# Performance work log

Hardware: AMD Instinct MI355X
Metric: run time of the kernel (lower is better)

Reference implementation:

```python
import jax, jax.numpy as jnp
import numpy as np

B, DIM, HID, K, G, MID = 1024, 384, 64, 8, 48, 128
EPS = 1e-06


def _gaussian_8x8():
    t = jnp.arange(K, dtype=jnp.float32) - 3.5
    g = jnp.exp(-(t[:, None] ** 2 + t[None, :] ** 2) / (2.0 * 2.0 ** 2))
    return g / g.sum()


def setup_inputs() -> dict:
    key = jax.random.key(0)
    ks = jax.random.split(key, 16)
    inp = {
        "x": jax.random.normal(ks[0], (B, DIM), dtype=jnp.float32),
        "W": jax.random.normal(ks[1], (DIM, HID), dtype=jnp.float32) * 0.02,
        "b": jax.random.normal(ks[2], (DIM, HID), dtype=jnp.float32) * 0.02,
        "patch_weight": _gaussian_8x8(),  # learnable 8x8, softmaxed in forward
        "pair_w1": jax.random.normal(ks[3], (G, G), dtype=jnp.float32) * 0.02,
        "pair_b1": jax.random.normal(ks[4], (G, G), dtype=jnp.float32) * 0.02,
        "pair_w2": jax.random.normal(ks[5], (G, G), dtype=jnp.float32) * 0.02,
        "pair_b2": jax.random.normal(ks[6], (G, G), dtype=jnp.float32) * 0.02,
        # nn.Linear(G, DIM)
        "proj_w": jax.random.normal(ks[7], (DIM, G), dtype=jnp.float32) * (1.0 / np.sqrt(G)),
        "proj_b": jax.random.normal(ks[8], (DIM,), dtype=jnp.float32) * 0.02,
        # nn.Linear(HID, MID)
        "down_w": jax.random.normal(ks[9], (MID, HID), dtype=jnp.float32) * (1.0 / np.sqrt(HID)),
        "down_b": jax.random.normal(ks[10], (MID,), dtype=jnp.float32) * 0.02,
        # nn.Linear(MID, HID)
        "up_w": jax.random.normal(ks[11], (HID, MID), dtype=jnp.float32) * (1.0 / np.sqrt(MID)),
        "up_b": jax.random.normal(ks[12], (HID,), dtype=jnp.float32) * 0.02,
    }
    return inp


def _leaky(v):
    return jnp.where(v >= 0, v, 0.01 * v)


def reference(x, W, b, patch_weight, pair_w1, pair_b1, pair_w2, pair_b2,
              proj_w, proj_b, down_w, down_b, up_w, up_b):
    # scale / inverse-bias GELU features: (B, DIM, HID)
    s = x[:, :, None]
    inv = 1.0 / (jnp.abs(s) + EPS)
    H = jax.nn.gelu(s * W[None] + inv * b[None], approximate=False)
    # Gram matrix over hidden dim: (B, DIM, DIM)
    P = jnp.einsum('bik,bjk->bij', H, H)
    # learnable gaussian patch pooling (softmax over flattened 8x8 weights)
    w = jax.nn.softmax(patch_weight.reshape(-1)).reshape(K, K)
    Pg = jnp.einsum('bgkhl,kl->bgh', P.reshape(-1, G, K, G, K), w)  # (B, G, G)
    # two elementwise gated leaky layers
    Pg = _leaky(Pg * pair_w1[None] + pair_b1[None])
    Pg = _leaky(Pg * pair_w2[None] + pair_b2[None])
    # softmax + nonlinear row reduction -> (B, G)
    row_soft = jax.nn.softmax(Pg, axis=-1)
    row_weights = (1.0 / (1.0 + row_soft ** 2)).sum(axis=-1)
    # project 48 -> 384, scale rows of H
    scales = row_weights @ proj_w.T + proj_b  # (B, DIM)
    H = H * scales[:, :, None]
    # tiny MLP on hidden dim
    z = _leaky(H @ down_w.T + down_b)
    z = _leaky(z @ up_w.T + up_b)
    return z
```

## Files before the change

kernel.cpp:

```cpp
#include <hip/hip_runtime.h>


#define EPSF 1e-6f

typedef __attribute__((ext_vector_type(8))) short bf16x8;
typedef __attribute__((ext_vector_type(4))) float f32x4;
typedef __attribute__((ext_vector_type(4))) unsigned short u16x4;

__device__ __forceinline__ unsigned short f2bf(float f) {
    union { float f; unsigned int u; } v; v.f = f;
    unsigned int r = v.u + 0x7fffu + ((v.u >> 16) & 1u);
    return (unsigned short)(r >> 16);
}
__device__ __forceinline__ float bf2f(unsigned short h) {
    union { unsigned int u; float f; } v; v.u = ((unsigned int)h) << 16;
    return v.f;
}
__device__ __forceinline__ float leaky(float v) { return fmaxf(v, 0.01f * v); }
__device__ __forceinline__ int key8(int r) { return (r ^ (r >> 3)) & 7; }
__device__ __forceinline__ float gelu_f(float u) {
    float t = u * (1.5957691216f + 0.0713548163f * (u * u));
    float e = __expf(t);
    float r = __builtin_amdgcn_rcpf(e + 1.0f);
    return fmaf(-u, r, u);
}

__global__ void prep(const float* __restrict__ proj_w,
                     const float* __restrict__ down_w,
                     const float* __restrict__ up_w,
                     float* __restrict__ ws) {
    int idx = blockIdx.x * blockDim.x + threadIdx.x;
    unsigned short* wb = (unsigned short*)(ws + 18432);
    if (idx < 18432) {
        int i = idx / 48, g = idx % 48;
        ws[g * 384 + i] = proj_w[idx];
    } else if (idx < 26624) {
        int k = idx - 18432;
        wb[k] = f2bf(down_w[k]);
    } else if (idx < 34816) {
        int k = idx - 26624;
        wb[8192 + k] = f2bf(up_w[k]);
    }
}

__global__ __launch_bounds__(512, 4) void pg_scales(
    const float* __restrict__ x,
    const float* __restrict__ W,
    const float* __restrict__ bb,
    const float* __restrict__ patch_weight,
    const float* __restrict__ pw1, const float* __restrict__ pb1,
    const float* __restrict__ pw2, const float* __restrict__ pb2,
    const float* __restrict__ proj_b,
    float* __restrict__ ws)
{
    __shared__ __align__(16) unsigned short sH[24576];
    __shared__ __align__(16) unsigned short sRB[12288];
    __shared__ float sw[64];
    __shared__ float srw[48];

    const int t = threadIdx.x;
    const int b = blockIdx.x;
    const int wv = t >> 6, lane = t & 63, q = lane >> 4, r = lane & 15;
    const float* projT = ws;
    float* scales_g = ws + 26624;
    unsigned short* sM  = sRB;
    float* sPg = (float*)sRB;

    if (t < 64) {
        float p = patch_weight[t];
        float m = p;
        for (int o = 32; o > 0; o >>= 1) m = fmaxf(m, __shfl_xor(m, o));
        float e = __expf(p - m);
        float s = e;
        for (int o = 32; o > 0; o >>= 1) s += __shfl_xor(s, o);
        sw[t] = e * __builtin_amdgcn_rcpf(s);
    }

    for (int j = 0; j < 12; ++j) {
        int idx4 = j * 512 + t;
        int base = idx4 * 4;
        int i = base >> 6, c0 = base & 63;
        float4 w4 = ((const float4*)W)[idx4];
        float4 b4 = ((const float4*)bb)[idx4];
        float xi  = x[b * 384 + i];
        float inv = __builtin_amdgcn_rcpf(fabsf(xi) + EPSF);
        u16x4 hv;
        hv[0] = f2bf(gelu_f(fmaf(xi, w4.x, inv * b4.x)));
        hv[1] = f2bf(gelu_f(fmaf(xi, w4.y, inv * b4.y)));
        hv[2] = f2bf(gelu_f(fmaf(xi, w4.z, inv * b4.z)));
        hv[3] = f2bf(gelu_f(fmaf(xi, w4.w, inv * b4.w)));
        int cb = c0 >> 3, cc = c0 & 7;
        *(u16x4*)&sH[i * 64 + ((cb ^ key8(i)) << 3) + cc] = hv;
    }
    __syncthreads();

    f32x4 pacc  = {0.f, 0.f, 0.f, 0.f};
    f32x4 pacc8 = {0.f, 0.f, 0.f, 0.f};
    for (int hc = 0; hc < 2; ++hc) {
        if (t < 384) {
            const int cb = t & 3, lq = (t >> 2) & 1, g = t >> 3;
            float acc[4][8];
            #pragma unroll
            for (int a = 0; a < 4; ++a)
                #pragma unroll
                for (int cc = 0; cc < 8; ++cc) acc[a][cc] = 0.0f;
            #pragma unroll
            for (int k = 0; k < 8; ++k) {
                int i = g * 8 + k;
                int cbh = hc * 4 + cb;
                bf16x8 hv = *(const bf16x8*)&sH[i * 64 + ((cbh ^ key8(i)) << 3)];
                f32x4 w4 = *(const f32x4*)&sw[k * 8 + lq * 4];
                float hf[8];
                #pragma unroll
                for (int cc = 0; cc < 8; ++cc) hf[cc] = bf2f((unsigned short)hv[cc]);
                #pragma unroll
                for (int a = 0; a < 4; ++a)
                    #pragma unroll
                    for (int cc = 0; cc < 8; ++cc)
                        acc[a][cc] = fmaf(w4[a], hf[cc], acc[a][cc]);
            }
            #pragma unroll
            for (int a = 0; a < 4; ++a) {
                int l = lq * 4 + a;
                int cbl = l * 4 + cb;
                int cbs = (cbl & 24) | ((cbl ^ key8(g)) & 7);
                bf16x8 mv;
                #pragma unroll
                for (int cc = 0; cc < 8; ++cc) mv[cc] = (short)f2bf(acc[a][cc]);
                *(bf16x8*)&sM[g * 256 + (cbs << 3)] = mv;
            }
        }
        __syncthreads();
        {
            const int tg = wv / 3, th = wv % 3;
            #pragma unroll
            for (int ks = 0; ks < 8; ++ks) {
                int g = tg * 16 + r;
                int cbl = ks * 4 + q;
                int cbs = (cbl & 24) | ((cbl ^ key8(g)) & 7);
                bf16x8 av = *(const bf16x8*)&sM[g * 256 + (cbs << 3)];
                int i = (th * 16 + r) * 8 + ks;
                int cbh = hc * 4 + q;
                bf16x8 bv = *(const bf16x8*)&sH[i * 64 + ((cbh ^ key8(i)) << 3)];
                pacc = __builtin_amdgcn_mfma_f32_16x16x32_bf16(av, bv, pacc, 0, 0, 0);
            }
            if (wv == 7) {
                #pragma unroll
                for (int ks = 0; ks < 8; ++ks) {
                    int g = 32 + r;
                    int cbl = ks * 4 + q;
                    int cbs = (cbl & 24) | ((cbl ^ key8(g)) & 7);
                    bf16x8 av = *(const bf16x8*)&sM[g * 256 + (cbs << 3)];
                    int i = (32 + r) * 8 + ks;
                    int cbh = hc * 4 + q;
                    bf16x8 bv = *(const bf16x8*)&sH[i * 64 + ((cbh ^ key8(i)) << 3)];
                    pacc8 = __builtin_amdgcn_mfma_f32_16x16x32_bf16(av, bv, pacc8, 0, 0, 0);
                }
            }
        }
        __syncthreads();
    }

    {
        const int tg = wv / 3, th = wv % 3;
        #pragma unroll
        for (int reg = 0; reg < 4; ++reg) {
            int g = tg * 16 + q * 4 + reg;
            int h = th * 16 + r;
            int idx = g * 48 + h;
            float v = pacc[reg];
            v = leaky(fmaf(v, pw1[idx], pb1[idx]));
            v = leaky(fmaf(v, pw2[idx], pb2[idx]));
            sPg[g * 49 + h] = v;
        }
        if (wv == 7) {
            #pragma unroll
            for (int reg = 0; reg < 4; ++reg) {
                int g = 32 + q * 4 + reg;
                int h = 32 + r;
                int idx = g * 48 + h;
                float v = pacc8[reg];
                v = leaky(fmaf(v, pw1[idx], pb1[idx]));
                v = leaky(fmaf(v, pw2[idx], pb2[idx]));
                sPg[g * 49 + h] = v;
            }
        }
    }
    __syncthreads();

    if (wv < 6) {
        #pragma unroll
        for (int it = 0; it < 2; ++it) {
            int row = wv * 8 + it * 4 + (lane >> 4);
            int idx = lane & 15;
            const float* pr = &sPg[row * 49 + idx * 3];
            float v0 = pr[0], v1 = pr[1], v2 = pr[2];
            float m = fmaxf(v0, fmaxf(v1, v2));
            #pragma unroll
            for (int o = 8; o > 0; o >>= 1) m = fmaxf(m, __shfl_xor(m, o));
            float e0 = __expf(v0 - m), e1 = __expf(v1 - m), e2 = __expf(v2 - m);
            float s = e0 + e1 + e2;
            #pragma unroll
            for (int o = 8; o > 0; o >>= 1) s += __shfl_xor(s, o);
            float rs = __builtin_amdgcn_rcpf(s);
            float p0 = e0 * rs, p1 = e1 * rs, p2 = e2 * rs;
            float rw = __builtin_amdgcn_rcpf(fmaf(p0, p0, 1.0f))
                     + __builtin_amdgcn_rcpf(fmaf(p1, p1, 1.0f))
                     + __builtin_amdgcn_rcpf(fmaf(p2, p2, 1.0f));
            #pragma unroll
            for (int o = 8; o > 0; o >>= 1) rw += __shfl_xor(rw, o);
            if (idx == 0) srw[row] = rw;
        }
    }
    __syncthreads();

    if (t < 384) {
        float s = proj_b[t];
        #pragma unroll 4
        for (int g = 0; g < 48; ++g) s = fmaf(srw[g], projT[g * 384 + t], s);
        scales_g[b * 384 + t] = s;
    }
}

__global__ __launch_bounds__(512, 8) void ffn(
    const float* __restrict__ x,
    const float* __restrict__ W,
    const float* __restrict__ bb,
    const float* __restrict__ down_b,
    const float* __restrict__ up_b,
    const float* __restrict__ ws,
    float* __restrict__ out)
{
    __shared__ __align__(16) unsigned short sHc[6144];
    __shared__ __align__(16) unsigned short sZ1[12288];
    __shared__ float sSc[96];
    __shared__ float sDb[128];
    __shared__ float sUb[64];

    const int t = threadIdx.x;
    const int bid = blockIdx.x;
    const int b = bid >> 2, rt = bid & 3, r0 = rt * 96;
    const int wv = t >> 6, lane = t & 63, q = lane >> 4, r = lane & 15;
    const unsigned short* dwB = (const unsigned short*)(ws + 18432);
    const unsigned short* uwB = dwB + 8192;
    const float* scales_g = ws + 26624;

    #pragma unroll
    for (int j = 0; j < 3; ++j) {
        int idx4 = j * 512 + t;
        int ir = idx4 >> 4;
        int i  = r0 + ir;
        int f4 = idx4 & 15;
        float4 w4 = ((const float4*)W)[i * 16 + f4];
        float4 b4 = ((const float4*)bb)[i * 16 + f4];
        float xi  = x[b * 384 + i];
        float inv = __builtin_amdgcn_rcpf(fabsf(xi) + EPSF);
        u16x4 hv;
        hv[0] = f2bf(gelu_f(fmaf(xi, w4.x, inv * b4.x)));
        hv[1] = f2bf(gelu_f(fmaf(xi, w4.y, inv * b4.y)));
        hv[2] = f2bf(gelu_f(fmaf(xi, w4.z, inv * b4.z)));
        hv[3] = f2bf(gelu_f(fmaf(xi, w4.w, inv * b4.w)));
        int c0 = f4 * 4;
        int cb = c0 >> 3, cc = c0 & 7;
        *(u16x4*)&sHc[ir * 64 + ((cb ^ key8(ir)) << 3) + cc] = hv;
    }
    if (t < 128) sDb[t] = down_b[t];
    else if (t < 192) sUb[t - 128] = up_b[t - 128];
    else if (t >= 416) sSc[t - 416] = scales_g[b * 384 + r0 + (t - 416)];
    __syncthreads();

    const int mg = wv >> 2, ng = wv & 3;
    f32x4 zacc[3][2];
    #pragma unroll
    for (int a = 0; a < 3; ++a)
        #pragma unroll
        for (int e = 0; e < 2; ++e) zacc[a][e] = (f32x4){0.f, 0.f, 0.f, 0.f};
    #pragma unroll
    for (int ks = 0; ks < 2; ++ks) {
        int cb = ks * 4 + q;
        bf16x8 af[3];
        #pragma unroll
        for (int a = 0; a < 3; ++a) {
            int ir = (mg * 3 + a) * 16 + r;
            af[a] = *(const bf16x8*)&sHc[ir * 64 + ((cb ^ key8(ir)) << 3)];
        }
        #pragma unroll
        for (int e = 0; e < 2; ++e) {
            int n = (ng * 2 + e) * 16 + r;
            bf16x8 bv = *(const bf16x8*)&dwB[n * 64 + cb * 8];
            #pragma unroll
            for (int a = 0; a < 3; ++a)
                zacc[a][e] = __builtin_amdgcn_mfma_f32_16x16x32_bf16(af[a], bv, zacc[a][e], 0, 0, 0);
        }
    }
    #pragma unroll
    for (int a = 0; a < 3; ++a) {
        #pragma unroll
        for (int e = 0; e < 2; ++e) {
            #pragma unroll
            for (int reg = 0; reg < 4; ++reg) {
                int rl = (mg * 3 + a) * 16 + q * 4 + reg;
                int m = (ng * 2 + e) * 16 + r;
                float v = leaky(fmaf(zacc[a][e][reg], sSc[rl], sDb[m]));
                int cb2 = m >> 3;
                int cbs2 = (cb2 & 8) | ((cb2 ^ key8(rl)) & 7);
                sZ1[rl * 128 + (cbs2 << 3) + (m & 7)] = f2bf(v);
            }
        }
    }
    __syncthreads();

    {
        const int grp = wv >> 2, nt = wv & 3;
        f32x4 oacc[3];
        #pragma unroll
        for (int a = 0; a < 3; ++a) oacc[a] = (f32x4){0.f, 0.f, 0.f, 0.f};
        #pragma unroll
        for (int ks = 0; ks < 4; ++ks) {
            int cb = ks * 4 + q;
            int p = nt * 16 + r;
            bf16x8 bv = *(const bf16x8*)&uwB[p * 128 + cb * 8];
            #pragma unroll
            for (int a = 0; a < 3; ++a) {
                int rl = (grp * 3 + a) * 16 + r;
                int cbsA = (cb & 8) | ((cb ^ key8(rl)) & 7);
                bf16x8 av = *(const bf16x8*)&sZ1[rl * 128 + (cbsA << 3)];
                oacc[a] = __builtin_amdgcn_mfma_f32_16x16x32_bf16(av, bv, oacc[a], 0, 0, 0);
            }
        }
        #pragma unroll
        for (int a = 0; a < 3; ++a) {
            #pragma unroll
            for (int reg = 0; reg < 4; ++reg) {
                int i = r0 + (grp * 3 + a) * 16 + q * 4 + reg;
                int cp = nt * 16 + r;
                out[(b * 384 + i) * 64 + cp] = leaky(oacc[a][reg] + sUb[cp]);
            }
        }
    }
}

extern "C" void kernel_launch(void* const* d_in, const int* in_sizes, int n_in,
                              void* d_out, int out_size, void* d_ws, size_t ws_size,
                              hipStream_t stream) {
    const float* x      = (const float*)d_in[0];
    const float* W      = (const float*)d_in[1];
    const float* bb     = (const float*)d_in[2];
    const float* pw     = (const float*)d_in[3];
    const float* pw1    = (const float*)d_in[4];
    const float* pb1    = (const float*)d_in[5];
    const float* pw2    = (const float*)d_in[6];
    const float* pb2    = (const float*)d_in[7];
    const float* proj_w = (const float*)d_in[8];
    const float* proj_b = (const float*)d_in[9];
    const float* down_w = (const float*)d_in[10];
    const float* down_b = (const float*)d_in[11];
    const float* up_w   = (const float*)d_in[12];
    const float* up_b   = (const float*)d_in[13];
    float* out = (float*)d_out;
    float* ws  = (float*)d_ws;

    prep<<<(34816 + 255) / 256, 256, 0, stream>>>(proj_w, down_w, up_w, ws);
    pg_scales<<<1024, 512, 0, stream>>>(x, W, bb, pw, pw1, pb1, pw2, pb2,
                                        proj_b, ws);
    ffn<<<4096, 512, 0, stream>>>(x, W, bb, down_b, up_b, ws, out);
}
```

Measured before the change: 213.6 us.

## Add precomputed bf16 H buffer path and fused single-kernel fallback

When the workspace is large enough, a new h_gen kernel computes the GELU features H once in bf16 into global memory. pg2 and ffn2 then load H from that buffer instead of recomputing it. When the workspace is too small, a fused_main kernel computes H once per batch element and runs the Gram pooling, scales and MLP in one block, which avoids the extra launch and the recomputation of H. The buffered path adds about 48MB of global traffic for writing and reading H. The fused path keeps 4 waves of FFN per block serially inside one large block.

```diff
diff --git a/kernel.cpp b/kernel.cpp
--- a/kernel.cpp
+++ b/kernel.cpp
@@ -6,6 +6,9 @@
 typedef __attribute__((ext_vector_type(8))) short bf16x8;
 typedef __attribute__((ext_vector_type(4))) float f32x4;
 typedef __attribute__((ext_vector_type(4))) unsigned short u16x4;
+
+#define HG_OFF 419840
+#define WS_NEED_BYTES (419840ull * 4ull + 50331648ull)
 
 __device__ __forceinline__ unsigned short f2bf(float f) {
     union { float f; unsigned int u; } v; v.f = f;
@@ -43,10 +46,54 @@
     }
 }
 
-__global__ __launch_bounds__(512, 4) void pg_scales(
+__global__ __launch_bounds__(512) void h_gen(
     const float* __restrict__ x,
     const float* __restrict__ W,
     const float* __restrict__ bb,
+    float* __restrict__ ws)
+{
+    __shared__ float sWc[6144];
+    __shared__ float sBc[6144];
+
+    const int t = threadIdx.x;
+    const int bid = blockIdx.x;
+    const int rc = bid & 3, bg = bid >> 2;
+    const int r0 = rc * 96;
+    unsigned short* Hgp = (unsigned short*)(ws + HG_OFF);
+
+    #pragma unroll
+    for (int j = 0; j < 3; ++j) {
+        int idx4 = j * 512 + t;
+        ((float4*)sWc)[idx4] = ((const float4*)(W + r0 * 64))[idx4];
+        ((float4*)sBc)[idx4] = ((const float4*)(bb + r0 * 64))[idx4];
+    }
+    __syncthreads();
+
+    for (int nb = 0; nb < 16; ++nb) {
+        int b = bg * 16 + nb;
+        #pragma unroll
+        for (int j = 0; j < 3; ++j) {
+            int idx4 = j * 512 + t;
+            int ir = idx4 >> 4;
+            int i  = r0 + ir;
+            int f4 = idx4 & 15;
+            float4 w4 = ((const float4*)sWc)[idx4];
+            float4 b4 = ((const float4*)sBc)[idx4];
+            float xi  = x[b * 384 + i];
+            float inv = __builtin_amdgcn_rcpf(fabsf(xi) + EPSF);
+            u16x4 hv;
+            hv[0] = f2bf(gelu_f(fmaf(xi, w4.x, inv * b4.x)));
+            hv[1] = f2bf(gelu_f(fmaf(xi, w4.y, inv * b4.y)));
+            hv[2] = f2bf(gelu_f(fmaf(xi, w4.z, inv * b4.z)));
+            hv[3] = f2bf(gelu_f(fmaf(xi, w4.w, inv * b4.w)));
+            int c0 = f4 * 4;
+            int cb = c0 >> 3, cc = c0 & 7;
+            *(u16x4*)&Hgp[(size_t)b * 24576 + i * 64 + ((cb ^ key8(i)) << 3) + cc] = hv;
+        }
+    }
+}
+
+__global__ __launch_bounds__(512, 4) void pg2(
     const float* __restrict__ patch_weight,
     const float* __restrict__ pw1, const float* __restrict__ pb1,
     const float* __restrict__ pw2, const float* __restrict__ pb2,
@@ -63,6 +110,7 @@
     const int wv = t >> 6, lane = t & 63, q = lane >> 4, r = lane & 15;
     const float* projT = ws;
     float* scales_g = ws + 26624;
+    const unsigned short* Hb = (const unsigned short*)(ws + HG_OFF) + (size_t)b * 24576;
     unsigned short* sM  = sRB;
     float* sPg = (float*)sRB;
 
@@ -76,6 +124,281 @@
         sw[t] = e * __builtin_amdgcn_rcpf(s);
     }
 
+    #pragma unroll
+    for (int j = 0; j < 6; ++j) {
+        int idx = j * 512 + t;
+        *(bf16x8*)&sH[idx * 8] = *(const bf16x8*)&Hb[idx * 8];
+    }
+    __syncthreads();
+
+    f32x4 pacc  = {0.f, 0.f, 0.f, 0.f};
+    f32x4 pacc8 = {0.f, 0.f, 0.f, 0.f};
+    for (int hc = 0; hc < 2; ++hc) {
+        if (t < 384) {
+            const int cb = t & 3, lq = (t >> 2) & 1, g = t >> 3;
+            float acc[4][8];
+            #pragma unroll
+            for (int a = 0; a < 4; ++a)
+                #pragma unroll
+                for (int cc = 0; cc < 8; ++cc) acc[a][cc] = 0.0f;
+            #pragma unroll
+            for (int k = 0; k < 8; ++k) {
+                int i = g * 8 + k;
+                int cbh = hc * 4 + cb;
+                bf16x8 hv = *(const bf16x8*)&sH[i * 64 + ((cbh ^ key8(i)) << 3)];
+                f32x4 w4 = *(const f32x4*)&sw[k * 8 + lq * 4];
+                float hf[8];
+                #pragma unroll
+                for (int cc = 0; cc < 8; ++cc) hf[cc] = bf2f((unsigned short)hv[cc]);
+                #pragma unroll
+                for (int a = 0; a < 4; ++a)
+                    #pragma unroll
+                    for (int cc = 0; cc < 8; ++cc)
+                        acc[a][cc] = fmaf(w4[a], hf[cc], acc[a][cc]);
+            }
+            #pragma unroll
+            for (int a = 0; a < 4; ++a) {
+                int l = lq * 4 + a;
+                int cbl = l * 4 + cb;
+                int cbs = (cbl & 24) | ((cbl ^ key8(g)) & 7);
+                bf16x8 mv;
+                #pragma unroll
+                for (int cc = 0; cc < 8; ++cc) mv[cc] = (short)f2bf(acc[a][cc]);
+                *(bf16x8*)&sM[g * 256 + (cbs << 3)] = mv;
+            }
+        }
+        __syncthreads();
+        {
+            const int tg = wv / 3, th = wv % 3;
+            #pragma unroll
+            for (int ks = 0; ks < 8; ++ks) {
+                int g = tg * 16 + r;
+                int cbl = ks * 4 + q;
+                int cbs = (cbl & 24) | ((cbl ^ key8(g)) & 7);
+                bf16x8 av = *(const bf16x8*)&sM[g * 256 + (cbs << 3)];
+                int i = (th * 16 + r) * 8 + ks;
+                int cbh = hc * 4 + q;
+                bf16x8 bv = *(const bf16x8*)&sH[i * 64 + ((cbh ^ key8(i)) << 3)];
+                pacc = __builtin_amdgcn_mfma_f32_16x16x32_bf16(av, bv, pacc, 0, 0, 0);
+            }
+            if (wv == 7) {
+                #pragma unroll
+                for (int ks = 0; ks < 8; ++ks) {
+                    int g = 32 + r;
+                    int cbl = ks * 4 + q;
+                    int cbs = (cbl & 24) | ((cbl ^ key8(g)) & 7);
+                    bf16x8 av = *(const bf16x8*)&sM[g * 256 + (cbs << 3)];
+                    int i = (32 + r) * 8 + ks;
+                    int cbh = hc * 4 + q;
+                    bf16x8 bv = *(const bf16x8*)&sH[i * 64 + ((cbh ^ key8(i)) << 3)];
+                    pacc8 = __builtin_amdgcn_mfma_f32_16x16x32_bf16(av, bv, pacc8, 0, 0, 0);
+                }
+            }
+        }
+        __syncthreads();
+    }
+
+    {
+        const int tg = wv / 3, th = wv % 3;
+        #pragma unroll
+        for (int reg = 0; reg < 4; ++reg) {
+            int g = tg * 16 + q * 4 + reg;
+            int h = th * 16 + r;
+            int idx = g * 48 + h;
+            float v = pacc[reg];
+            v = leaky(fmaf(v, pw1[idx], pb1[idx]));
+            v = leaky(fmaf(v, pw2[idx], pb2[idx]));
+            sPg[g * 49 + h] = v;
+        }
+        if (wv == 7) {
+            #pragma unroll
+            for (int reg = 0; reg < 4; ++reg) {
+                int g = 32 + q * 4 + reg;
+                int h = 32 + r;
+                int idx = g * 48 + h;
+                float v = pacc8[reg];
+                v = leaky(fmaf(v, pw1[idx], pb1[idx]));
+                v = leaky(fmaf(v, pw2[idx], pb2[idx]));
+                sPg[g * 49 + h] = v;
+            }
+        }
+    }
+    __syncthreads();
+
+    if (wv < 6) {
+        #pragma unroll
+        for (int it = 0; it < 2; ++it) {
+            int row = wv * 8 + it * 4 + (lane >> 4);
+            int idx = lane & 15;
+            const float* pr = &sPg[row * 49 + idx * 3];
+            float v0 = pr[0], v1 = pr[1], v2 = pr[2];
+            float m = fmaxf(v0, fmaxf(v1, v2));
+            #pragma unroll
+            for (int o = 8; o > 0; o >>= 1) m = fmaxf(m, __shfl_xor(m, o));
+            float e0 = __expf(v0 - m), e1 = __expf(v1 - m), e2 = __expf(v2 - m);
+            float s = e0 + e1 + e2;
+            #pragma unroll
+            for (int o = 8; o > 0; o >>= 1) s += __shfl_xor(s, o);
+            float rs = __builtin_amdgcn_rcpf(s);
+            float p0 = e0 * rs, p1 = e1 * rs, p2 = e2 * rs;
+            float rw = __builtin_amdgcn_rcpf(fmaf(p0, p0, 1.0f))
+                     + __builtin_amdgcn_rcpf(fmaf(p1, p1, 1.0f))
+                     + __builtin_amdgcn_rcpf(fmaf(p2, p2, 1.0f));
+            #pragma unroll
+            for (int o = 8; o > 0; o >>= 1) rw += __shfl_xor(rw, o);
+            if (idx == 0) srw[row] = rw;
+        }
+    }
+    __syncthreads();
+
+    if (t < 384) {
+        float s = proj_b[t];
+        #pragma unroll 4
+        for (int g = 0; g < 48; ++g) s = fmaf(srw[g], projT[g * 384 + t], s);
+        scales_g[b * 384 + t] = s;
+    }
+}
+
+__global__ __launch_bounds__(512, 8) void ffn2(
+    const float* __restrict__ down_b,
+    const float* __restrict__ up_b,
+    const float* __restrict__ ws,
+    float* __restrict__ out)
+{
+    __shared__ __align__(16) unsigned short sHc[6144];
+    __shared__ __align__(16) unsigned short sZ1[12288];
+    __shared__ float sSc[96];
+    __shared__ float sDb[128];
+    __shared__ float sUb[64];
+
+    const int t = threadIdx.x;
+    const int bid = blockIdx.x;
+    const int b = bid >> 2, rt = bid & 3, r0 = rt * 96;
+    const int wv = t >> 6, lane = t & 63, q = lane >> 4, r = lane & 15;
+    const unsigned short* dwB = (const unsigned short*)(ws + 18432);
+    const unsigned short* uwB = dwB + 8192;
+    const float* scales_g = ws + 26624;
+    const unsigned short* Hb = (const unsigned short*)(ws + HG_OFF)
+                             + (size_t)b * 24576 + r0 * 64;
+
+    for (int idx = t; idx < 768; idx += 512)
+        *(bf16x8*)&sHc[idx * 8] = *(const bf16x8*)&Hb[idx * 8];
+    if (t < 128) sDb[t] = down_b[t];
+    else if (t < 192) sUb[t - 128] = up_b[t - 128];
+    else if (t >= 416) sSc[t - 416] = scales_g[b * 384 + r0 + (t - 416)];
+    __syncthreads();
+
+    const int mg = wv >> 2, ng = wv & 3;
+    f32x4 zacc[3][2];
+    #pragma unroll
+    for (int a = 0; a < 3; ++a)
+        #pragma unroll
+        for (int e = 0; e < 2; ++e) zacc[a][e] = (f32x4){0.f, 0.f, 0.f, 0.f};
+    #pragma unroll
+    for (int ks = 0; ks < 2; ++ks) {
+        int cb = ks * 4 + q;
+        bf16x8 af[3];
+        #pragma unroll
+        for (int a = 0; a < 3; ++a) {
+            int ir = (mg * 3 + a) * 16 + r;
+            af[a] = *(const bf16x8*)&sHc[ir * 64 + ((cb ^ key8(r0 + ir)) << 3)];
+        }
+        #pragma unroll
+        for (int e = 0; e < 2; ++e) {
+            int n = (ng * 2 + e) * 16 + r;
+            bf16x8 bv = *(const bf16x8*)&dwB[n * 64 + cb * 8];
+            #pragma unroll
+            for (int a = 0; a < 3; ++a)
+                zacc[a][e] = __builtin_amdgcn_mfma_f32_16x16x32_bf16(af[a], bv, zacc[a][e], 0, 0, 0);
+        }
+    }
+    #pragma unroll
+    for (int a = 0; a < 3; ++a) {
+        #pragma unroll
+        for (int e = 0; e < 2; ++e) {
+            #pragma unroll
+            for (int reg = 0; reg < 4; ++reg) {
+                int rl = (mg * 3 + a) * 16 + q * 4 + reg;
+                int m = (ng * 2 + e) * 16 + r;
+                float v = leaky(fmaf(zacc[a][e][reg], sSc[rl], sDb[m]));
+                int cb2 = m >> 3;
+                int cbs2 = (cb2 & 8) | ((cb2 ^ key8(rl)) & 7);
+                sZ1[rl * 128 + (cbs2 << 3) + (m & 7)] = f2bf(v);
+            }
+        }
+    }
+    __syncthreads();
+
+    {
+        const int grp = wv >> 2, nt = wv & 3;
+        f32x4 oacc[3];
+        #pragma unroll
+        for (int a = 0; a < 3; ++a) oacc[a] = (f32x4){0.f, 0.f, 0.f, 0.f};
+        #pragma unroll
+        for (int ks = 0; ks < 4; ++ks) {
+            int cb = ks * 4 + q;
+            int p = nt * 16 + r;
+            bf16x8 bv = *(const bf16x8*)&uwB[p * 128 + cb * 8];
+            #pragma unroll
+            for (int a = 0; a < 3; ++a) {
+                int rl = (grp * 3 + a) * 16 + r;
+                int cbsA = (cb & 8) | ((cb ^ key8(rl)) & 7);
+                bf16x8 av = *(const bf16x8*)&sZ1[rl * 128 + (cbsA << 3)];
+                oacc[a] = __builtin_amdgcn_mfma_f32_16x16x32_bf16(av, bv, oacc[a], 0, 0, 0);
+            }
+        }
+        #pragma unroll
+        for (int a = 0; a < 3; ++a) {
+            #pragma unroll
+            for (int reg = 0; reg < 4; ++reg) {
+                int i = r0 + (grp * 3 + a) * 16 + q * 4 + reg;
+                int cp = nt * 16 + r;
+                out[(b * 384 + i) * 64 + cp] = leaky(oacc[a][reg] + sUb[cp]);
+            }
+        }
+    }
+}
+
+__global__ __launch_bounds__(512, 4) void fused_main(
+    const float* __restrict__ x,
+    const float* __restrict__ W,
+    const float* __restrict__ bb,
+    const float* __restrict__ patch_weight,
+    const float* __restrict__ pw1, const float* __restrict__ pb1,
+    const float* __restrict__ pw2, const float* __restrict__ pb2,
+    const float* __restrict__ proj_b,
+    const float* __restrict__ down_b,
+    const float* __restrict__ up_b,
+    const float* __restrict__ ws,
+    float* __restrict__ out)
+{
+    __shared__ __align__(16) unsigned short sH[24576];
+    __shared__ __align__(16) unsigned short sRB[12288];
+    __shared__ float sw[64];
+    __shared__ float srw[48];
+    __shared__ float sScale[384];
+    __shared__ float sDb[128];
+    __shared__ float sUb[64];
+
+    const int t = threadIdx.x;
+    const int b = blockIdx.x;
+    const int wv = t >> 6, lane = t & 63, q = lane >> 4, r = lane & 15;
+    const float* projT = ws;
+    const unsigned short* dwB = (const unsigned short*)(ws + 18432);
+    const unsigned short* uwB = dwB + 8192;
+    unsigned short* sM  = sRB;
+    float* sPg = (float*)sRB;
+    unsigned short* sZ1 = sRB;
+
+    if (t < 64) {
+        float p = patch_weight[t];
+        float m = p;
+        for (int o = 32; o > 0; o >>= 1) m = fmaxf(m, __shfl_xor(m, o));
+        float e = __expf(p - m);
+        float s = e;
+        for (int o = 32; o > 0; o >>= 1) s += __shfl_xor(s, o);
+        sw[t] = e * __builtin_amdgcn_rcpf(s);
+    }
     for (int j = 0; j < 12; ++j) {
         int idx4 = j * 512 + t;
         int base = idx4 * 4;
@@ -129,6 +452,10 @@
                 for (int cc = 0; cc < 8; ++cc) mv[cc] = (short)f2bf(acc[a][cc]);
                 *(bf16x8*)&sM[g * 256 + (cbs << 3)] = mv;
             }
+        } else if (hc == 0) {
+            int tt = t - 384;
+            if (tt < 128) sDb[tt] = down_b[tt];
+            if (tt < 64)  sUb[tt] = up_b[tt];
         }
         __syncthreads();
         {
@@ -160,7 +487,6 @@
         }
         __syncthreads();
     }
-
     {
         const int tg = wv / 3, th = wv % 3;
         #pragma unroll
@@ -187,7 +513,6 @@
         }
     }
     __syncthreads();
-
     if (wv < 6) {
         #pragma unroll
         for (int it = 0; it < 2; ++it) {
@@ -213,128 +538,70 @@
         }
     }
     __syncthreads();
-
-    if (t < 384) {
-        float s = proj_b[t];
-        #pragma unroll 4
-        for (int g = 0; g < 48; ++g) s = fmaf(srw[g], projT[g * 384 + t], s);
-        scales_g[b * 384 + t] = s;
-    }
-}
-
-__global__ __launch_bounds__(512, 8) void ffn(
-    const float* __restrict__ x,
-    const float* __restrict__ W,
-    const float* __restrict__ bb,
-    const float* __restrict__ down_b,
-    const float* __restrict__ up_b,
-    const float* __restrict__ ws,
-    float* __restrict__ out)
-{
-    __shared__ __align__(16) unsigned short sHc[6144];
-    __shared__ __align__(16) unsigned short sZ1[12288];
-    __shared__ float sSc[96];
-    __shared__ float sDb[128];
-    __shared__ float sUb[64];
-
-    const int t = threadIdx.x;
-    const int bid = blockIdx.x;
-    const int b = bid >> 2, rt = bid & 3, r0 = rt * 96;
-    const int wv = t >> 6, lane = t & 63, q = lane >> 4, r = lane & 15;
-    const unsigned short* dwB = (const unsigned short*)(ws + 18432);
-    const unsigned short* uwB = dwB + 8192;
-    const float* scales_g = ws + 26624;
-
-    #pragma unroll
-    for (int j = 0; j < 3; ++j) {
-        int idx4 = j * 512 + t;
-        int ir = idx4 >> 4;
-        int i  = r0 + ir;
-        int f4 = idx4 & 15;
-        float4 w4 = ((const float4*)W)[i * 16 + f4];
-        float4 b4 = ((const float4*)bb)[i * 16 + f4];
-        float xi  = x[b * 384 + i];
-        float inv = __builtin_amdgcn_rcpf(fabsf(xi) + EPSF);
-        u16x4 hv;
-        hv[0] = f2bf(gelu_f(fmaf(xi, w4.x, inv * b4.x)));
-        hv[1] = f2bf(gelu_f(fmaf(xi, w4.y, inv * b4.y)));
-        hv[2] = f2bf(gelu_f(fmaf(xi, w4.z, inv * b4.z)));
-        hv[3] = f2bf(gelu_f(fmaf(xi, w4.w, inv * b4.w)));
-        int c0 = f4 * 4;
-        int cb = c0 >> 3, cc = c0 & 7;
-        *(u16x4*)&sHc[ir * 64 + ((cb ^ key8(ir)) << 3) + cc] = hv;
-    }
-    if (t < 128) sDb[t] = down_b[t];
-    else if (t < 192) sUb[t - 128] = up_b[t - 128];
-    else if (t >= 416) sSc[t - 416] = scales_g[b * 384 + r0 + (t - 416)];
-    __syncthreads();
-
-    const int mg = wv >> 2, ng = wv & 3;
-    f32x4 zacc[3][2];
-    #pragma unroll
-    for (int a = 0; a < 3; ++a)
-        #pragma unroll
-        for (int e = 0; e < 2; ++e) zacc[a][e] = (f32x4){0.f, 0.f, 0.f, 0.f};
-    #pragma unroll
-    for (int ks = 0; ks < 2; ++ks) {
-        int cb = ks * 4 + q;
-        bf16x8 af[3];
-        #pragma unroll
-        for (int a = 0; a < 3; ++a) {
-            int ir = (mg * 3 + a) * 16 + r;
-            af[a] = *(const bf16x8*)&sHc[ir * 64 + ((cb ^ key8(ir)) << 3)];
-        }
-        #pragma unroll
-        for (int e = 0; e < 2; ++e) {
-            int n = (ng * 2 + e) * 16 + r;
+    #pragma unroll 1
+    for (int rt = 0; rt < 4; ++rt) {
+        const int r0 = rt * 96;
+        if (rt == 0 && t < 384) {
+            float s = proj_b[t];
+            #pragma unroll 4
+            for (int g = 0; g < 48; ++g) s = fmaf(srw[g], projT[g * 384 + t], s);
+            sScale[t] = s;
+        }
+        f32x4 zacc[6];
+        #pragma unroll
+        for (int a = 0; a < 6; ++a) zacc[a] = (f32x4){0.f, 0.f, 0.f, 0.f};
+        #pragma unroll
+        for (int ks = 0; ks < 2; ++ks) {
+            int cb = ks * 4 + q;
+            int n = wv * 16 + r;
             bf16x8 bv = *(const bf16x8*)&dwB[n * 64 + cb * 8];
             #pragma unroll
-            for (int a = 0; a < 3; ++a)
-                zacc[a][e] = __builtin_amdgcn_mfma_f32_16x16x32_bf16(af[a], bv, zacc[a][e], 0, 0, 0);
-        }
-    }
-    #pragma unroll
-    for (int a = 0; a < 3; ++a) {
-        #pragma unroll
-        for (int e = 0; e < 2; ++e) {
+            for (int a = 0; a < 6; ++a) {
+                int i = r0 + a * 16 + r;
+                bf16x8 av = *(const bf16x8*)&sH[i * 64 + ((cb ^ key8(i)) << 3)];
+                zacc[a] = __builtin_amdgcn_mfma_f32_16x16x32_bf16(av, bv, zacc[a], 0, 0, 0);
+            }
+        }
+        __syncthreads();
+        #pragma unroll
+        for (int a = 0; a < 6; ++a) {
             #pragma unroll
             for (int reg = 0; reg < 4; ++reg) {
-                int rl = (mg * 3 + a) * 16 + q * 4 + reg;
-                int m = (ng * 2 + e) * 16 + r;
-                float v = leaky(fmaf(zacc[a][e][reg], sSc[rl], sDb[m]));
+                int rl = a * 16 + q * 4 + reg;
+                int m = wv * 16 + r;
+                float v = leaky(fmaf(zacc[a][reg], sScale[r0 + rl], sDb[m]));
                 int cb2 = m >> 3;
                 int cbs2 = (cb2 & 8) | ((cb2 ^ key8(rl)) & 7);
                 sZ1[rl * 128 + (cbs2 << 3) + (m & 7)] = f2bf(v);
             }
         }
-    }
-    __syncthreads();
-
-    {
-        const int grp = wv >> 2, nt = wv & 3;
-        f32x4 oacc[3];
-        #pragma unroll
-        for (int a = 0; a < 3; ++a) oacc[a] = (f32x4){0.f, 0.f, 0.f, 0.f};
-        #pragma unroll
-        for (int ks = 0; ks < 4; ++ks) {
-            int cb = ks * 4 + q;
-            int p = nt * 16 + r;
-            bf16x8 bv = *(const bf16x8*)&uwB[p * 128 + cb * 8];
+        __syncthreads();
+        {
+            const int grp = wv >> 2, nt = wv & 3;
+            f32x4 oacc[3];
+            #pragma unroll
+            for (int a = 0; a < 3; ++a) oacc[a] = (f32x4){0.f, 0.f, 0.f, 0.f};
+            #pragma unroll
+            for (int ks = 0; ks < 4; ++ks) {
+                int cb = ks * 4 + q;
+                int p = nt * 16 + r;
+                bf16x8 bv = *(const bf16x8*)&uwB[p * 128 + cb * 8];
+                #pragma unroll
+                for (int a = 0; a < 3; ++a) {
+                    int rl = (grp * 3 + a) * 16 + r;
+                    int cbsA = (cb & 8) | ((cb ^ key8(rl)) & 7);
+                    bf16x8 av = *(const bf16x8*)&sZ1[rl * 128 + (cbsA << 3)];
+                    oacc[a] = __builtin_amdgcn_mfma_f32_16x16x32_bf16(av, bv, oacc[a], 0, 0, 0);
+                }
+            }
             #pragma unroll
             for (int a = 0; a < 3; ++a) {
-                int rl = (grp * 3 + a) * 16 + r;
-                int cbsA = (cb & 8) | ((cb ^ key8(rl)) & 7);
-                bf16x8 av = *(const bf16x8*)&sZ1[rl * 128 + (cbsA << 3)];
-                oacc[a] = __builtin_amdgcn_mfma_f32_16x16x32_bf16(av, bv, oacc[a], 0, 0, 0);
-            }
-        }
-        #pragma unroll
-        for (int a = 0; a < 3; ++a) {
-            #pragma unroll
-            for (int reg = 0; reg < 4; ++reg) {
-                int i = r0 + (grp * 3 + a) * 16 + q * 4 + reg;
-                int cp = nt * 16 + r;
-                out[(b * 384 + i) * 64 + cp] = leaky(oacc[a][reg] + sUb[cp]);
+                #pragma unroll
+                for (int reg = 0; reg < 4; ++reg) {
+                    int i = r0 + (grp * 3 + a) * 16 + q * 4 + reg;
+                    int cp = nt * 16 + r;
+                    out[(b * 384 + i) * 64 + cp] = leaky(oacc[a][reg] + sUb[cp]);
+                }
             }
         }
     }
@@ -361,7 +628,12 @@
     float* ws  = (float*)d_ws;
 
     prep<<<(34816 + 255) / 256, 256, 0, stream>>>(proj_w, down_w, up_w, ws);
-    pg_scales<<<1024, 512, 0, stream>>>(x, W, bb, pw, pw1, pb1, pw2, pb2,
-                                        proj_b, ws);
-    ffn<<<4096, 512, 0, stream>>>(x, W, bb, down_b, up_b, ws, out);
-}
+    if (ws_size >= WS_NEED_BYTES) {
+        h_gen<<<256, 512, 0, stream>>>(x, W, bb, ws);
+        pg2<<<1024, 512, 0, stream>>>(pw, pw1, pb1, pw2, pb2, proj_b, ws);
+        ffn2<<<4096, 512, 0, stream>>>(down_b, up_b, ws, out);
+    } else {
+        fused_main<<<1024, 512, 0, stream>>>(x, W, bb, pw, pw1, pb1, pw2, pb2,
+                                             proj_b, down_b, up_b, ws, out);
+    }
+}
```

Measured after the change: 222.8 us. 4.3% more time.
